# Kernel tuning notes

Measured on AMD Instinct MI355X. Metric: run time of the kernel, lower is better.

The kernel has to match this reference:

```python
import jax, jax.numpy as jnp
import numpy as np

N = 30000
E = 480000
F_IN = 16
HID = 64
HEADS = 2
D = HID // HEADS
L = 2
NEG_SLOPE = 0.2


def _edge_softmax(alpha, dst, num_nodes):
    # alpha: [E, HEADS]; softmax over edges sharing the same destination node
    amax = jax.ops.segment_max(alpha, dst, num_segments=num_nodes)
    ex = jnp.exp(alpha - amax[dst])
    den = jax.ops.segment_sum(ex, dst, num_segments=num_nodes)
    return ex / (den[dst] + 1e-16)


def _han_edge(x_src, x_dst, ei, a_src, a_dst, n_dst):
    # x_src: [N_src, HEADS, D], x_dst: [N_dst, HEADS, D], ei: [2, E]
    src, dst = ei[0], ei[1]
    a_s = jnp.einsum('nhd,hd->nh', x_src, a_src)
    a_d = jnp.einsum('nhd,hd->nh', x_dst, a_dst)
    alpha = jax.nn.leaky_relu(a_s[src] + a_d[dst], NEG_SLOPE)  # [E, HEADS]
    alpha = _edge_softmax(alpha, dst, n_dst)
    msg = x_src[src] * alpha[..., None]                        # [E, HEADS, D]
    out = jax.ops.segment_sum(msg, dst, num_segments=n_dst)
    return jax.nn.relu(out.reshape(n_dst, HID))


def _group(xs, q, kw, kb):
    # semantic (cross-relation) attention; xs: list of [N, HID]
    out = jnp.stack(xs)                           # [T, N, HID]
    k = jnp.tanh(out @ kw + kb).mean(axis=1)      # [T, HID]
    attn = jax.nn.softmax(jnp.einsum('f,tf->t', q, k))
    return jnp.einsum('t,tnf->nf', attn, out)


def setup_inputs() -> dict:
    key = jax.random.key(0)
    ks = jax.random.split(key, 24)
    s = 0.1
    f32 = jnp.float32
    return {
        'x_job': jax.random.normal(ks[0], (N, F_IN), f32),
        'x_machine': jax.random.normal(ks[1], (N, F_IN), f32),
        'edge_index_jm': jax.random.randint(ks[2], (2, E), 0, N),
        'edge_index_mj': jax.random.randint(ks[3], (2, E), 0, N),
        'edge_index_jj': jax.random.randint(ks[4], (2, E), 0, N),
        'enc_w_job': jax.random.normal(ks[5], (F_IN, HID), f32) * s,
        'enc_b_job': jax.random.normal(ks[6], (HID,), f32) * s,
        'enc_w_machine': jax.random.normal(ks[7], (F_IN, HID), f32) * s,
        'enc_b_machine': jax.random.normal(ks[8], (HID,), f32) * s,
        'proj_w': jax.random.normal(ks[9], (L, 2, HID, HID), f32) * s,
        'proj_b': jax.random.normal(ks[10], (L, 2, HID), f32) * s,
        'att_src': jax.random.normal(ks[11], (L, 3, HEADS, D), f32) * s,
        'att_dst': jax.random.normal(ks[12], (L, 3, HEADS, D), f32) * s,
        'klin_w': jax.random.normal(ks[13], (L, HID, HID), f32) * s,
        'klin_b': jax.random.normal(ks[14], (L, HID), f32) * s,
        'q_sem': jax.random.normal(ks[15], (L, HID), f32) * s,
        'lin0_w': jax.random.normal(ks[16], (HID, HID), f32) * s,
        'lin0_b': jax.random.normal(ks[17], (HID,), f32) * s,
        'linout_w': jax.random.normal(ks[18], (HID, 16), f32) * s,
        'linout_b': jax.random.normal(ks[19], (16,), f32) * s,
        'linv_w': jax.random.normal(ks[20], (HID, 1), f32) * s,
        'linv_b': jax.random.normal(ks[21], (1,), f32) * s,
    }


def reference(x_job, x_machine, edge_index_jm, edge_index_mj, edge_index_jj,
              enc_w_job, enc_b_job, enc_w_machine, enc_b_machine,
              proj_w, proj_b, att_src, att_dst, klin_w, klin_b, q_sem,
              lin0_w, lin0_b, linout_w, linout_b, linv_w, linv_b):
    # per-node-type encoder: Linear + relu_
    xj = jax.nn.relu(x_job @ enc_w_job + enc_b_job)          # [N, HID]
    xm = jax.nn.relu(x_machine @ enc_w_machine + enc_b_machine)
    for l in range(L):
        pj = (xj @ proj_w[l, 0] + proj_b[l, 0]).reshape(N, HEADS, D)
        pm = (xm @ proj_w[l, 1] + proj_b[l, 1]).reshape(N, HEADS, D)
        # edge-type order follows edge_index_dict iteration: jm, mj, jj
        out_jm = _han_edge(pj, pm, edge_index_jm, att_src[l, 0], att_dst[l, 0], N)
        out_mj = _han_edge(pm, pj, edge_index_mj, att_src[l, 1], att_dst[l, 1], N)
        out_jj = _han_edge(pj, pj, edge_index_jj, att_src[l, 2], att_dst[l, 2], N)
        xj = _group([out_mj, out_jj], q_sem[l], klin_w[l], klin_b[l])
        xm = _group([out_jm], q_sem[l], klin_w[l], klin_b[l])
    full_x = jnp.concatenate([xj, xm], axis=0)               # [2N, HID]
    value = (full_x @ linv_w + linv_b).mean()
    h = full_x @ lin0_w + lin0_b
    action = jnp.tanh(h @ linout_w + linout_b)               # [2N, 16]
    return action, value
```

## Files before the change

kernel.cpp:

```cpp
#include <hip/hip_runtime.h>
#include <math.h>


#define GEMM_GRID 1024
#define KRED_GRID 256
#define BUCKET_SHIFT 6
#define BUCKET_NODES 64
#define BUCKET_CAP 1536
#define BIN_CHUNK 2048

__device__ __forceinline__ float4 ld4(const float* __restrict__ p, int idx4)
{
    return ((const float4*)p)[idx4];
}

__device__ __forceinline__ float halfred(float v)
{
#pragma unroll
    for (int off = 16; off; off >>= 1) v += __shfl_xor(v, off);
    return v;
}

__device__ __forceinline__ float2 sem_attn(const float* __restrict__ kacc,
                                           const float* __restrict__ qsem,
                                           float inv_n, int lane)
{
    float qc = qsem[lane];
    float v0 = qc * kacc[lane] * inv_n;
    float v1 = qc * kacc[64 + lane] * inv_n;
#pragma unroll
    for (int off = 32; off; off >>= 1) {
        v0 += __shfl_xor(v0, off);
        v1 += __shfl_xor(v1, off);
    }
    float m = fmaxf(v0, v1);
    float e0 = __expf(v0 - m), e1 = __expf(v1 - m);
    float inv = 1.f / (e0 + e1);
    return {e0 * inv, e1 * inv};
}

struct ProjSide {
    const float* x0; const float* x1;
    const float* kacc; const float* qsem; float inv_n;
    const float* W; const float* b; float* p;
    const float* a0v; float* o0; const float* a1v; float* o1;
    const float* a2v; float* o2; const float* a3v; float* o3;
};

__global__ __launch_bounds__(256, 4) void proj2_kernel(ProjSide sa, ProjSide sb, int n)
{
    const ProjSide S = blockIdx.y ? sb : sa;
    __shared__ __align__(16) float xs[16][64];
    int tid = threadIdx.x, lane = tid & 63, wid = tid >> 6;
    float Wreg[64];
#pragma unroll
    for (int k = 0; k < 64; k++) Wreg[k] = S.W[k * 64 + lane];
    float bc = S.b[lane];
    float a0c = S.o0 ? S.a0v[lane] : 0.f;
    float a1c = S.o1 ? S.a1v[lane] : 0.f;
    float a2c = S.o2 ? S.a2v[lane] : 0.f;
    float a3c = S.o3 ? S.a3v[lane] : 0.f;
    float ca0 = 0.f, ca1 = 0.f;
    if (S.x1) {
        float2 at = sem_attn(S.kacc, S.qsem, S.inv_n, lane);
        ca0 = at.x; ca1 = at.y;
    }
    int qn = tid >> 4, qq = tid & 15;
    for (int base = blockIdx.x * 16; base < n; base += gridDim.x * 16) {
        __syncthreads();
        int node = base + qn;
        if (node < n) {
            float4 xq;
            if (S.x1) {
                float4 u = ld4(S.x0, node * 16 + qq), v = ld4(S.x1, node * 16 + qq);
                xq.x = ca0 * u.x + ca1 * v.x; xq.y = ca0 * u.y + ca1 * v.y;
                xq.z = ca0 * u.z + ca1 * v.z; xq.w = ca0 * u.w + ca1 * v.w;
            } else {
                xq = ld4(S.x0, node * 16 + qq);
            }
            *(float4*)&xs[qn][qq * 4] = xq;
        }
        __syncthreads();
#pragma unroll
        for (int nd = 0; nd < 4; nd++) {
            int nc = base + wid * 4 + nd;
            if (nc >= n) break;
            float acc = bc;
#pragma unroll
            for (int k4 = 0; k4 < 16; k4++) {
                float4 xv = *(const float4*)&xs[wid * 4 + nd][k4 * 4];
                acc = fmaf(xv.x, Wreg[4 * k4 + 0], acc);
                acc = fmaf(xv.y, Wreg[4 * k4 + 1], acc);
                acc = fmaf(xv.z, Wreg[4 * k4 + 2], acc);
                acc = fmaf(xv.w, Wreg[4 * k4 + 3], acc);
            }
            S.p[nc * 64 + lane] = acc;
            int h = lane >> 5;
            if (S.o0) { float v = halfred(acc * a0c); if ((lane & 31) == 0) S.o0[nc * 2 + h] = v; }
            if (S.o1) { float v = halfred(acc * a1c); if ((lane & 31) == 0) S.o1[nc * 2 + h] = v; }
            if (S.o2) { float v = halfred(acc * a2c); if ((lane & 31) == 0) S.o2[nc * 2 + h] = v; }
            if (S.o3) { float v = halfred(acc * a3c); if ((lane & 31) == 0) S.o3[nc * 2 + h] = v; }
        }
    }
}

struct EncSide {
    const float* x; const float* We; const float* be;
    const float* W; const float* b; float* p;
    const float* a0v; float* o0; const float* a1v; float* o1;
    const float* a2v; float* o2; const float* a3v; float* o3;
};

__global__ __launch_bounds__(256, 4) void encproj2_kernel(EncSide sa, EncSide sb, int n)
{
    const EncSide S = blockIdx.y ? sb : sa;
    __shared__ __align__(16) float xs[16][16];
    __shared__ __align__(16) float es[16][64];
    int tid = threadIdx.x, lane = tid & 63, wid = tid >> 6;
    float Ereg[16];
#pragma unroll
    for (int k = 0; k < 16; k++) Ereg[k] = S.We[k * 64 + lane];
    float Wreg[64];
#pragma unroll
    for (int k = 0; k < 64; k++) Wreg[k] = S.W[k * 64 + lane];
    float ebc = S.be[lane], bc = S.b[lane];
    float a0c = S.o0 ? S.a0v[lane] : 0.f;
    float a1c = S.o1 ? S.a1v[lane] : 0.f;
    float a2c = S.o2 ? S.a2v[lane] : 0.f;
    float a3c = S.o3 ? S.a3v[lane] : 0.f;
    for (int base = blockIdx.x * 16; base < n; base += gridDim.x * 16) {
        __syncthreads();
        if (tid < 64) {
            int nn = tid >> 2, q = tid & 3;
            int node = base + nn;
            if (node < n) *(float4*)&xs[nn][q * 4] = ld4(S.x, node * 4 + q);
        }
        __syncthreads();
#pragma unroll
        for (int nd = 0; nd < 4; nd++) {
            int nc = base + wid * 4 + nd;
            if (nc >= n) break;
            float a = ebc;
#pragma unroll
            for (int k4 = 0; k4 < 4; k4++) {
                float4 xv = *(const float4*)&xs[wid * 4 + nd][k4 * 4];
                a = fmaf(xv.x, Ereg[4 * k4 + 0], a);
                a = fmaf(xv.y, Ereg[4 * k4 + 1], a);
                a = fmaf(xv.z, Ereg[4 * k4 + 2], a);
                a = fmaf(xv.w, Ereg[4 * k4 + 3], a);
            }
            es[wid * 4 + nd][lane] = fmaxf(a, 0.f);
        }
        __syncthreads();
#pragma unroll
        for (int nd = 0; nd < 4; nd++) {
            int nc = base + wid * 4 + nd;
            if (nc >= n) break;
            float acc = bc;
#pragma unroll
            for (int k4 = 0; k4 < 16; k4++) {
                float4 xv = *(const float4*)&es[wid * 4 + nd][k4 * 4];
                acc = fmaf(xv.x, Wreg[4 * k4 + 0], acc);
                acc = fmaf(xv.y, Wreg[4 * k4 + 1], acc);
                acc = fmaf(xv.z, Wreg[4 * k4 + 2], acc);
                acc = fmaf(xv.w, Wreg[4 * k4 + 3], acc);
            }
            S.p[nc * 64 + lane] = acc;
            int h = lane >> 5;
            if (S.o0) { float v = halfred(acc * a0c); if ((lane & 31) == 0) S.o0[nc * 2 + h] = v; }
            if (S.o1) { float v = halfred(acc * a1c); if ((lane & 31) == 0) S.o1[nc * 2 + h] = v; }
            if (S.o2) { float v = halfred(acc * a2c); if ((lane & 31) == 0) S.o2[nc * 2 + h] = v; }
            if (S.o3) { float v = halfred(acc * a3c); if ((lane & 31) == 0) S.o3[nc * 2 + h] = v; }
        }
    }
}

__global__ __launch_bounds__(256) void bin_kernel(
    const int* __restrict__ s0, const int* __restrict__ s1, const int* __restrict__ s2,
    const int* __restrict__ d0, const int* __restrict__ d1, const int* __restrict__ d2,
    int* __restrict__ cursor, int* __restrict__ binned, int e, int nb)
{
    int ty = blockIdx.y;
    const int* s = ty == 0 ? s0 : (ty == 1 ? s1 : s2);
    const int* d = ty == 0 ? d0 : (ty == 1 ? d1 : d2);
    __shared__ int cnt[512], rbase[512];
    int tid = threadIdx.x;
    for (int i = tid; i < nb; i += 256) cnt[i] = 0;
    __syncthreads();
    int beg = blockIdx.x * BIN_CHUNK;
    int end = beg + BIN_CHUNK; if (end > e) end = e;
    for (int i = beg + tid; i < end; i += 256)
        atomicAdd(&cnt[d[i] >> BUCKET_SHIFT], 1);
    __syncthreads();
    for (int i = tid; i < nb; i += 256) {
        rbase[i] = atomicAdd(&cursor[ty * nb + i], cnt[i]);
        cnt[i] = 0;
    }
    __syncthreads();
    int* bb = binned + (size_t)ty * nb * BUCKET_CAP;
    for (int i = beg + tid; i < end; i += 256) {
        int dv = d[i], b = dv >> BUCKET_SHIFT;
        int slot = rbase[b] + atomicAdd(&cnt[b], 1);
        if (slot < BUCKET_CAP)
            bb[b * BUCKET_CAP + slot] = (s[i] << BUCKET_SHIFT) | (dv & (BUCKET_NODES - 1));
    }
}

__global__ void bucketscan_kernel(const int* __restrict__ cursor,
                                  int* __restrict__ bbase, int nb)
{
    int ty = blockIdx.x;
    const int* c = cursor + (size_t)ty * nb;
    int* o = bbase + (size_t)ty * nb;
    int lane = threadIdx.x;
    int carry = 0;
    for (int base = 0; base < nb; base += 64) {
        int i = base + lane;
        int v = (i < nb) ? c[i] : 0;
        int incl = v;
#pragma unroll
        for (int off = 1; off < 64; off <<= 1) {
            int u = __shfl_up(incl, off);
            if (lane >= off) incl += u;
        }
        if (i < nb) o[i] = carry + incl - v;
        carry += __shfl(incl, 63);
    }
}

__global__ __launch_bounds__(256) void bucket_kernel(
    const int* __restrict__ cursor, const int* __restrict__ bbase,
    const int* __restrict__ binned,
    int* __restrict__ rowptr, int* __restrict__ rowend, int* __restrict__ colsrc,
    int n, int nb, int e)
{
    int ty = blockIdx.y, b = blockIdx.x;
    __shared__ int stage[BUCKET_CAP];
    __shared__ int ncnt[64], nexcl[64], ncur[64];
    int tid = threadIdx.x;
    int cnt = cursor[ty * nb + b]; if (cnt > BUCKET_CAP) cnt = BUCKET_CAP;
    int base = bbase[ty * nb + b];
    const int* bb = binned + ((size_t)ty * nb + b) * BUCKET_CAP;
    if (tid < 64) ncnt[tid] = 0;
    __syncthreads();
    for (int i = tid; i < cnt; i += 256) {
        int v = bb[i];
        stage[i] = v;
        atomicAdd(&ncnt[v & (BUCKET_NODES - 1)], 1);
    }
    __syncthreads();
    if (tid < 64) {
        int v = ncnt[tid];
        int incl = v;
#pragma unroll
        for (int off = 1; off < 64; off <<= 1) {
            int u = __shfl_up(incl, off);
            if (tid >= off) incl += u;
        }
        int excl = incl - v;
        nexcl[tid] = excl;
        ncur[tid] = 0;
        int node = (b << BUCKET_SHIFT) + tid;
        if (node < n) {
            rowptr[(size_t)ty * n + node] = base + excl;
            rowend[(size_t)ty * n + node] = base + excl + v;
        }
    }
    __syncthreads();
    int* cs = colsrc + (size_t)ty * e;
    for (int i = tid; i < cnt; i += 256) {
        int v = stage[i];
        int dl = v & (BUCKET_NODES - 1);
        int pos = nexcl[dl] + atomicAdd(&ncur[dl], 1);
        cs[base + pos] = v >> BUCKET_SHIFT;
    }
}

struct AggSide {
    const int* rp; const int* re; const int* cs;
    const float* xsrc; const float* as; const float* ad;
    float* out;
};

__global__ __launch_bounds__(256, 8) void agg3_kernel(AggSide A0, AggSide A1, AggSide A2, int n)
{
    const AggSide A = blockIdx.y == 0 ? A0 : (blockIdx.y == 1 ? A1 : A2);
    __shared__ int ebs[4][32];
    __shared__ float ebw[4][2][32];
    int tid = threadIdx.x;
    int lane = tid & 63, wid = tid >> 6;
    int node = blockIdx.x * 4 + wid;
    if (node >= n) return;
    int l32 = lane & 31;
    int hh = lane >> 5;
    int g = lane >> 4;
    int q = lane & 15;
    int hq = q >> 3;
    int beg = A.rp[node], end = A.re[node];
    float ad = A.ad[node * 2 + hh];
    float den = 0.f;
    float4 acc = {0.f, 0.f, 0.f, 0.f};
    int* es = ebs[wid];
    float* ew = ebw[wid][0];
    for (int c = beg; c < end; c += 32) {
        int cnt = end - c; if (cnt > 32) cnt = 32;
        int sl = A.cs[c + (l32 < cnt ? l32 : 0)];
        float w = 0.f;
        if (l32 < cnt) {
            float a = A.as[sl * 2 + hh] + ad;
            a = (a > 0.f) ? a : 0.2f * a;
            w = __expf(a);
        }
        den += w;
        if (lane < 32) es[l32] = sl;
        ew[hh * 32 + l32] = w;
        int iters = (cnt + 3) >> 2;
        int it = 0;
        for (; it + 4 <= iters; it += 4) {
            int e0 = it * 4 + g;
            int s0 = es[e0], s1 = es[e0 + 4], s2 = es[e0 + 8], s3 = es[e0 + 12];
            float w0 = ew[hq * 32 + e0],     w1 = ew[hq * 32 + e0 + 4];
            float w2 = ew[hq * 32 + e0 + 8], w3 = ew[hq * 32 + e0 + 12];
            float4 x0 = ld4(A.xsrc, s0 * 16 + q);
            float4 x1 = ld4(A.xsrc, s1 * 16 + q);
            float4 x2 = ld4(A.xsrc, s2 * 16 + q);
            float4 x3 = ld4(A.xsrc, s3 * 16 + q);
            acc.x = fmaf(w0, x0.x, acc.x); acc.y = fmaf(w0, x0.y, acc.y);
            acc.z = fmaf(w0, x0.z, acc.z); acc.w = fmaf(w0, x0.w, acc.w);
            acc.x = fmaf(w1, x1.x, acc.x); acc.y = fmaf(w1, x1.y, acc.y);
            acc.z = fmaf(w1, x1.z, acc.z); acc.w = fmaf(w1, x1.w, acc.w);
            acc.x = fmaf(w2, x2.x, acc.x); acc.y = fmaf(w2, x2.y, acc.y);
            acc.z = fmaf(w2, x2.z, acc.z); acc.w = fmaf(w2, x2.w, acc.w);
            acc.x = fmaf(w3, x3.x, acc.x); acc.y = fmaf(w3, x3.y, acc.y);
            acc.z = fmaf(w3, x3.z, acc.z); acc.w = fmaf(w3, x3.w, acc.w);
        }
        for (; it < iters; it++) {
            int e0 = it * 4 + g;
            int s0 = es[e0];
            float w0 = ew[hq * 32 + e0];
            float4 x0 = ld4(A.xsrc, s0 * 16 + q);
            acc.x = fmaf(w0, x0.x, acc.x); acc.y = fmaf(w0, x0.y, acc.y);
            acc.z = fmaf(w0, x0.z, acc.z); acc.w = fmaf(w0, x0.w, acc.w);
        }
    }
    acc.x += __shfl_xor(acc.x, 16);
    acc.y += __shfl_xor(acc.y, 16);
    acc.z += __shfl_xor(acc.z, 16);
    acc.w += __shfl_xor(acc.w, 16);
    acc.x += __shfl_xor(acc.x, 32);
    acc.y += __shfl_xor(acc.y, 32);
    acc.z += __shfl_xor(acc.z, 32);
    acc.w += __shfl_xor(acc.w, 32);
    float dtot = halfred(den);
    float dq = __shfl(dtot, (q >= 8) ? 32 : 0);
    if (g == 0) {
        float r = 1.f / (dq + 1e-16f);
        float4 o;
        o.x = fmaxf(acc.x * r, 0.f);
        o.y = fmaxf(acc.y * r, 0.f);
        o.z = fmaxf(acc.z * r, 0.f);
        o.w = fmaxf(acc.w * r, 0.f);
        *(float4*)&A.out[node * 64 + q * 4] = o;
    }
}

__global__ __launch_bounds__(256, 4) void kred2_kernel(
    const float* __restrict__ xin0, const float* __restrict__ xin1,
    const float* __restrict__ kw, const float* __restrict__ kb,
    float* __restrict__ kacc0, float* __restrict__ kacc1, int n)
{
    const float* xin = blockIdx.y ? xin1 : xin0;
    float* kacc = blockIdx.y ? kacc1 : kacc0;
    __shared__ __align__(16) float xs[16][64];
    __shared__ float red[256];
    int tid = threadIdx.x, lane = tid & 63, wid = tid >> 6;
    float Wreg[64];
#pragma unroll
    for (int k = 0; k < 64; k++) Wreg[k] = kw[k * 64 + lane];
    float bc = kb[lane];
    int qn = tid >> 4, qq = tid & 15;
    float kl = 0.f;
    for (int base = blockIdx.x * 16; base < n; base += gridDim.x * 16) {
        __syncthreads();
        int node = base + qn;
        if (node < n) *(float4*)&xs[qn][qq * 4] = ld4(xin, node * 16 + qq);
        __syncthreads();
#pragma unroll
        for (int nd = 0; nd < 4; nd++) {
            int nc = base + wid * 4 + nd;
            if (nc >= n) break;
            float acc = bc;
#pragma unroll
            for (int k4 = 0; k4 < 16; k4++) {
                float4 xv = *(const float4*)&xs[wid * 4 + nd][k4 * 4];
                acc = fmaf(xv.x, Wreg[4 * k4 + 0], acc);
                acc = fmaf(xv.y, Wreg[4 * k4 + 1], acc);
                acc = fmaf(xv.z, Wreg[4 * k4 + 2], acc);
                acc = fmaf(xv.w, Wreg[4 * k4 + 3], acc);
            }
            kl += tanhf(acc);
        }
    }
    red[tid] = kl;
    __syncthreads();
    if (wid == 0) {
        float s = red[lane] + red[64 + lane] + red[128 + lane] + red[192 + lane];
        atomicAdd(&kacc[lane], s);
    }
}

__global__ __launch_bounds__(256, 4) void final_kernel(
    const float* __restrict__ t0, const float* __restrict__ t1,
    const float* __restrict__ kacc, const float* __restrict__ qsem, float inv_n,
    const float* __restrict__ xm,
    const float* __restrict__ w0, const float* __restrict__ b0,
    const float* __restrict__ w1, const float* __restrict__ b1,
    const float* __restrict__ wv,
    float* __restrict__ action, float* __restrict__ vsum, int n)
{
    __shared__ __align__(16) float xs[16][64];
    __shared__ __align__(16) float hs[4][4][68];
    __shared__ float W1s[1024];
    __shared__ float red[256];
    int tid = threadIdx.x, lane = tid & 63, wid = tid >> 6;
    int qn = tid >> 4, qq = tid & 15;
    float W0reg[64];
#pragma unroll
    for (int k = 0; k < 64; k++) W0reg[k] = w0[k * 64 + lane];
    float b0c = b0[lane], b1c = b1[lane & 15];
    float2 at = sem_attn(kacc, qsem, inv_n, lane);
    float ca0 = at.x, ca1 = at.y;
    float4 wvq = ld4(wv, qq);
    for (int i = tid; i < 1024; i += 256) W1s[i] = w1[i];
    float vloc = 0.f;
    int n2 = 2 * n;
    for (int base = blockIdx.x * 16; base < n2; base += gridDim.x * 16) {
        __syncthreads();
        int node = base + qn;
        if (node < n2) {
            float4 xq;
            if (node < n) {
                float4 u = ld4(t0, node * 16 + qq), v = ld4(t1, node * 16 + qq);
                xq.x = ca0 * u.x + ca1 * v.x; xq.y = ca0 * u.y + ca1 * v.y;
                xq.z = ca0 * u.z + ca1 * v.z; xq.w = ca0 * u.w + ca1 * v.w;
            } else {
                xq = ld4(xm, (node - n) * 16 + qq);
            }
            *(float4*)&xs[qn][qq * 4] = xq;
            vloc += xq.x * wvq.x + xq.y * wvq.y + xq.z * wvq.z + xq.w * wvq.w;
        }
        __syncthreads();
#pragma unroll
        for (int nd = 0; nd < 4; nd++) {
            int nc = base + wid * 4 + nd;
            if (nc >= n2) break;
            float acc = b0c;
#pragma unroll
            for (int k4 = 0; k4 < 16; k4++) {
                float4 xv = *(const float4*)&xs[wid * 4 + nd][k4 * 4];
                acc = fmaf(xv.x, W0reg[4 * k4 + 0], acc);
                acc = fmaf(xv.y, W0reg[4 * k4 + 1], acc);
                acc = fmaf(xv.z, W0reg[4 * k4 + 2], acc);
                acc = fmaf(xv.w, W0reg[4 * k4 + 3], acc);
            }
            hs[wid][nd][lane] = acc;
        }
        __syncthreads();
        int nd2 = lane >> 4, c2 = lane & 15;
        int nc2 = base + wid * 4 + nd2;
        if (nc2 < n2) {
            float acc2 = b1c;
#pragma unroll
            for (int k4 = 0; k4 < 16; k4++) {
                float4 hv = *(const float4*)&hs[wid][nd2][k4 * 4];
                acc2 = fmaf(hv.x, W1s[(4 * k4 + 0) * 16 + c2], acc2);
                acc2 = fmaf(hv.y, W1s[(4 * k4 + 1) * 16 + c2], acc2);
                acc2 = fmaf(hv.z, W1s[(4 * k4 + 2) * 16 + c2], acc2);
                acc2 = fmaf(hv.w, W1s[(4 * k4 + 3) * 16 + c2], acc2);
            }
            action[(size_t)nc2 * 16 + c2] = tanhf(acc2);
        }
    }
    red[tid] = vloc;
    __syncthreads();
    for (int s = 128; s; s >>= 1) {
        if (tid < s) red[tid] += red[tid + s];
        __syncthreads();
    }
    if (tid == 0) atomicAdd(vsum, red[0]);
}

__global__ void value_finish_kernel(const float* __restrict__ vsum,
                                    const float* __restrict__ vb,
                                    float* __restrict__ out, int twoN)
{
    if (threadIdx.x == 0 && blockIdx.x == 0)
        out[0] = vsum[0] / (float)twoN + vb[0];
}

extern "C" void kernel_launch(void* const* d_in, const int* in_sizes, int n_in,
                              void* d_out, int out_size, void* d_ws, size_t ws_size,
                              hipStream_t stream)
{
    const int N = in_sizes[0] / 16;
    const int E = in_sizes[2] / 2;
    const int NB = (N + BUCKET_NODES - 1) / BUCKET_NODES;

    auto f = [&](int i) { return (const float*)d_in[i]; };
    const float* x_job = f(0);
    const float* x_mac = f(1);
    const int* ei_jm = (const int*)d_in[2];
    const int* ei_mj = (const int*)d_in[3];
    const int* ei_jj = (const int*)d_in[4];
    const float* enc_wj = f(5);
    const float* enc_bj = f(6);
    const float* enc_wm = f(7);
    const float* enc_bm = f(8);
    const float* proj_w = f(9);
    const float* proj_b = f(10);
    const float* att_src = f(11);
    const float* att_dst = f(12);
    const float* klin_w = f(13);
    const float* klin_b = f(14);
    const float* q_sem = f(15);
    const float* lin0_w = f(16);
    const float* lin0_b = f(17);
    const float* lout_w = f(18);
    const float* lout_b = f(19);
    const float* linv_w = f(20);
    const float* linv_b = f(21);

    float* action = (float*)d_out;
    float* value_out = action + (size_t)2 * N * 16;

    char* base = (char*)d_ws;
    size_t off = 0;
    auto alloc = [&](size_t bytes) -> void* {
        void* p = base + off;
        off += (bytes + 255) & ~(size_t)255;
        return p;
    };
    int* cursor3 = (int*)alloc((size_t)3 * NB * 4);
    float* kacc = (float*)alloc(256 * 4);
    float* vsum = (float*)alloc(4);
    size_t zero_bytes = off;

    int* bbase3 = (int*)alloc((size_t)3 * NB * 4);
    int* rowptr3 = (int*)alloc((size_t)3 * N * 4);
    int* rowend3 = (int*)alloc((size_t)3 * N * 4);
    int* colsrc3 = (int*)alloc((size_t)3 * E * 4);
    float* pj = (float*)alloc((size_t)N * 64 * 4);
    float* pm = (float*)alloc((size_t)N * 64 * 4);
    float* out_jm0 = (float*)alloc((size_t)N * 64 * 4);
    float* out_jm1 = (float*)alloc((size_t)N * 64 * 4);
    float* out_mj = (float*)alloc((size_t)N * 64 * 4);
    float* out_jj = (float*)alloc((size_t)N * 64 * 4);
    float* as_jm = (float*)alloc((size_t)N * 2 * 4);
    float* ad_jm = (float*)alloc((size_t)N * 2 * 4);
    float* as_mj = (float*)alloc((size_t)N * 2 * 4);
    float* ad_mj = (float*)alloc((size_t)N * 2 * 4);
    float* as_jj = (float*)alloc((size_t)N * 2 * 4);
    float* ad_jj = (float*)alloc((size_t)N * 2 * 4);

    int* binned3 = (int*)pj;

    hipMemsetAsync(d_ws, 0, zero_bytes, stream);

    dim3 blk(256);

    int nchunks = (E + BIN_CHUNK - 1) / BIN_CHUNK;
    bin_kernel<<<dim3(nchunks, 3), blk, 0, stream>>>(
        ei_jm, ei_mj, ei_jj, ei_jm + E, ei_mj + E, ei_jj + E,
        cursor3, binned3, E, NB);
    bucketscan_kernel<<<3, 64, 0, stream>>>(cursor3, bbase3, NB);
    bucket_kernel<<<dim3(NB, 3), blk, 0, stream>>>(
        cursor3, bbase3, binned3, rowptr3, rowend3, colsrc3, N, NB, E);

    const int* rp0 = rowptr3;
    const int* rp1 = rowptr3 + N;
    const int* rp2 = rowptr3 + 2 * N;
    const int* re0 = rowend3;
    const int* re1 = rowend3 + N;
    const int* re2 = rowend3 + 2 * N;
    const int* cs0 = colsrc3;
    const int* cs1 = colsrc3 + E;
    const int* cs2 = colsrc3 + 2 * E;

    int ab = (N + 3) / 4;
    float* out_jm_l[2] = {out_jm0, out_jm1};
    float inv_n = 1.f / (float)N;

    for (int l = 0; l < 2; l++) {
        const float* pwj = proj_w + (size_t)(l * 2 + 0) * 4096;
        const float* pwm = proj_w + (size_t)(l * 2 + 1) * 4096;
        const float* pbj = proj_b + (l * 2 + 0) * 64;
        const float* pbm = proj_b + (l * 2 + 1) * 64;
        const float* as0 = att_src + (l * 3 + 0) * 64;
        const float* as1 = att_src + (l * 3 + 1) * 64;
        const float* as2 = att_src + (l * 3 + 2) * 64;
        const float* ad0 = att_dst + (l * 3 + 0) * 64;
        const float* ad1 = att_dst + (l * 3 + 1) * 64;
        const float* ad2 = att_dst + (l * 3 + 2) * 64;

        if (l == 0) {
            EncSide ja = {x_job, enc_wj, enc_bj, pwj, pbj, pj,
                          as0, as_jm, ad1, ad_mj, as2, as_jj, ad2, ad_jj};
            EncSide ma = {x_mac, enc_wm, enc_bm, pwm, pbm, pm,
                          ad0, ad_jm, as1, as_mj, nullptr, nullptr, nullptr, nullptr};
            encproj2_kernel<<<dim3(GEMM_GRID, 2), blk, 0, stream>>>(ja, ma, N);
        } else {
            ProjSide ja = {out_mj, out_jj, kacc, q_sem, inv_n, pwj, pbj, pj,
                           as0, as_jm, ad1, ad_mj, as2, as_jj, ad2, ad_jj};
            ProjSide ma = {out_jm0, nullptr, nullptr, nullptr, 0.f, pwm, pbm, pm,
                           ad0, ad_jm, as1, as_mj, nullptr, nullptr, nullptr, nullptr};
            proj2_kernel<<<dim3(GEMM_GRID, 2), blk, 0, stream>>>(ja, ma, N);
        }

        AggSide A0 = {rp0, re0, cs0, pj, as_jm, ad_jm, out_jm_l[l]};
        AggSide A1 = {rp1, re1, cs1, pm, as_mj, ad_mj, out_mj};
        AggSide A2 = {rp2, re2, cs2, pj, as_jj, ad_jj, out_jj};
        agg3_kernel<<<dim3(ab, 3), blk, 0, stream>>>(A0, A1, A2, N);

        const float* kw = klin_w + (size_t)l * 4096;
        const float* kb = klin_b + l * 64;
        float* k0 = kacc + l * 128;
        float* k1 = k0 + 64;
        kred2_kernel<<<dim3(KRED_GRID, 2), blk, 0, stream>>>(out_mj, out_jj, kw, kb, k0, k1, N);
    }

    final_kernel<<<GEMM_GRID * 2, blk, 0, stream>>>(out_mj, out_jj,
                                                    kacc + 128, q_sem + 64, inv_n,
                                                    out_jm1,
                                                    lin0_w, lin0_b, lout_w, lout_b, linv_w,
                                                    action, vsum, N);
    value_finish_kernel<<<1, 64, 0, stream>>>(vsum, linv_b, value_out, 2 * N);
}
```

Measured before the change: 361.0 us.

## Merge edge binning into encoder kernel and fold bucket scan into bucket kernel

```diff
diff --git a/kernel.cpp b/kernel.cpp
--- a/kernel.cpp
+++ b/kernel.cpp
@@ -3,6 +3,7 @@
 
 
 #define GEMM_GRID 1024
+#define ENCB 1024
 #define KRED_GRID 256
 #define BUCKET_SHIFT 6
 #define BUCKET_NODES 64
@@ -111,9 +112,8 @@
     const float* a2v; float* o2; const float* a3v; float* o3;
 };
 
-__global__ __launch_bounds__(256, 4) void encproj2_kernel(EncSide sa, EncSide sb, int n)
-{
-    const EncSide S = blockIdx.y ? sb : sa;
+__device__ __forceinline__ void encproj_body(const EncSide& S, int bx, int nblk, int n)
+{
     __shared__ __align__(16) float xs[16][16];
     __shared__ __align__(16) float es[16][64];
     int tid = threadIdx.x, lane = tid & 63, wid = tid >> 6;
@@ -128,7 +128,7 @@
     float a1c = S.o1 ? S.a1v[lane] : 0.f;
     float a2c = S.o2 ? S.a2v[lane] : 0.f;
     float a3c = S.o3 ? S.a3v[lane] : 0.f;
-    for (int base = blockIdx.x * 16; base < n; base += gridDim.x * 16) {
+    for (int base = bx * 16; base < n; base += nblk * 16) {
         __syncthreads();
         if (tid < 64) {
             int nn = tid >> 2, q = tid & 3;
@@ -175,19 +175,15 @@
     }
 }
 
-__global__ __launch_bounds__(256) void bin_kernel(
-    const int* __restrict__ s0, const int* __restrict__ s1, const int* __restrict__ s2,
-    const int* __restrict__ d0, const int* __restrict__ d1, const int* __restrict__ d2,
-    int* __restrict__ cursor, int* __restrict__ binned, int e, int nb)
-{
-    int ty = blockIdx.y;
-    const int* s = ty == 0 ? s0 : (ty == 1 ? s1 : s2);
-    const int* d = ty == 0 ? d0 : (ty == 1 ? d1 : d2);
+__device__ __forceinline__ void bin_body(const int* __restrict__ s, const int* __restrict__ d,
+                                         int* __restrict__ cursor, int* __restrict__ binned,
+                                         int ty, int cx, int e, int nb)
+{
     __shared__ int cnt[512], rbase[512];
     int tid = threadIdx.x;
     for (int i = tid; i < nb; i += 256) cnt[i] = 0;
     __syncthreads();
-    int beg = blockIdx.x * BIN_CHUNK;
+    int beg = cx * BIN_CHUNK;
     int end = beg + BIN_CHUNK; if (end > e) end = e;
     for (int i = beg + tid; i < end; i += 256)
         atomicAdd(&cnt[d[i] >> BUCKET_SHIFT], 1);
@@ -206,43 +202,44 @@
     }
 }
 
-__global__ void bucketscan_kernel(const int* __restrict__ cursor,
-                                  int* __restrict__ bbase, int nb)
-{
-    int ty = blockIdx.x;
-    const int* c = cursor + (size_t)ty * nb;
-    int* o = bbase + (size_t)ty * nb;
-    int lane = threadIdx.x;
-    int carry = 0;
-    for (int base = 0; base < nb; base += 64) {
-        int i = base + lane;
-        int v = (i < nb) ? c[i] : 0;
-        int incl = v;
-#pragma unroll
-        for (int off = 1; off < 64; off <<= 1) {
-            int u = __shfl_up(incl, off);
-            if (lane >= off) incl += u;
-        }
-        if (i < nb) o[i] = carry + incl - v;
-        carry += __shfl(incl, 63);
+__global__ __launch_bounds__(256) void phase1_kernel(
+    EncSide sa, EncSide sb, int n,
+    const int* __restrict__ s0, const int* __restrict__ s1, const int* __restrict__ s2,
+    const int* __restrict__ d0, const int* __restrict__ d1, const int* __restrict__ d2,
+    int* __restrict__ cursor, int* __restrict__ binned, int e, int nb, int binb)
+{
+    int bid = blockIdx.x;
+    if (bid < 2 * ENCB) {
+        encproj_body(bid >= ENCB ? sb : sa, bid & (ENCB - 1), ENCB, n);
+    } else {
+        int r = bid - 2 * ENCB;
+        int ty = r / binb, cx = r % binb;
+        const int* s = ty == 0 ? s0 : (ty == 1 ? s1 : s2);
+        const int* d = ty == 0 ? d0 : (ty == 1 ? d1 : d2);
+        bin_body(s, d, cursor, binned, ty, cx, e, nb);
     }
 }
 
 __global__ __launch_bounds__(256) void bucket_kernel(
-    const int* __restrict__ cursor, const int* __restrict__ bbase,
-    const int* __restrict__ binned,
+    const int* __restrict__ cursor, const int* __restrict__ binned,
     int* __restrict__ rowptr, int* __restrict__ rowend, int* __restrict__ colsrc,
     int n, int nb, int e)
 {
     int ty = blockIdx.y, b = blockIdx.x;
     __shared__ int stage[BUCKET_CAP];
     __shared__ int ncnt[64], nexcl[64], ncur[64];
-    int tid = threadIdx.x;
+    __shared__ int wpart[4];
+    int tid = threadIdx.x, lane = tid & 63, wid = tid >> 6;
+    int part = 0;
+    for (int i = tid; i < b; i += 256) part += cursor[ty * nb + i];
+#pragma unroll
+    for (int off = 32; off; off >>= 1) part += __shfl_xor(part, off);
+    if (lane == 0) wpart[wid] = part;
     int cnt = cursor[ty * nb + b]; if (cnt > BUCKET_CAP) cnt = BUCKET_CAP;
-    int base = bbase[ty * nb + b];
     const int* bb = binned + ((size_t)ty * nb + b) * BUCKET_CAP;
     if (tid < 64) ncnt[tid] = 0;
     __syncthreads();
+    int base = wpart[0] + wpart[1] + wpart[2] + wpart[3];
     for (int i = tid; i < cnt; i += 256) {
         int v = bb[i];
         stage[i] = v;
@@ -545,10 +542,10 @@
     float* vsum = (float*)alloc(4);
     size_t zero_bytes = off;
 
-    int* bbase3 = (int*)alloc((size_t)3 * NB * 4);
     int* rowptr3 = (int*)alloc((size_t)3 * N * 4);
     int* rowend3 = (int*)alloc((size_t)3 * N * 4);
     int* colsrc3 = (int*)alloc((size_t)3 * E * 4);
+    int* binned3 = (int*)alloc((size_t)3 * NB * BUCKET_CAP * 4);
     float* pj = (float*)alloc((size_t)N * 64 * 4);
     float* pm = (float*)alloc((size_t)N * 64 * 4);
     float* out_jm0 = (float*)alloc((size_t)N * 64 * 4);
@@ -562,19 +559,9 @@
     float* as_jj = (float*)alloc((size_t)N * 2 * 4);
     float* ad_jj = (float*)alloc((size_t)N * 2 * 4);
 
-    int* binned3 = (int*)pj;
-
     hipMemsetAsync(d_ws, 0, zero_bytes, stream);
 
     dim3 blk(256);
-
-    int nchunks = (E + BIN_CHUNK - 1) / BIN_CHUNK;
-    bin_kernel<<<dim3(nchunks, 3), blk, 0, stream>>>(
-        ei_jm, ei_mj, ei_jj, ei_jm + E, ei_mj + E, ei_jj + E,
-        cursor3, binned3, E, NB);
-    bucketscan_kernel<<<3, 64, 0, stream>>>(cursor3, bbase3, NB);
-    bucket_kernel<<<dim3(NB, 3), blk, 0, stream>>>(
-        cursor3, bbase3, binned3, rowptr3, rowend3, colsrc3, N, NB, E);
 
     const int* rp0 = rowptr3;
     const int* rp1 = rowptr3 + N;
@@ -587,6 +574,7 @@
     const int* cs2 = colsrc3 + 2 * E;
 
     int ab = (N + 3) / 4;
+    int binb = (E + BIN_CHUNK - 1) / BIN_CHUNK;
     float* out_jm_l[2] = {out_jm0, out_jm1};
     float inv_n = 1.f / (float)N;
 
@@ -607,7 +595,11 @@
                           as0, as_jm, ad1, ad_mj, as2, as_jj, ad2, ad_jj};
             EncSide ma = {x_mac, enc_wm, enc_bm, pwm, pbm, pm,
                           ad0, ad_jm, as1, as_mj, nullptr, nullptr, nullptr, nullptr};
-            encproj2_kernel<<<dim3(GEMM_GRID, 2), blk, 0, stream>>>(ja, ma, N);
+            phase1_kernel<<<2 * ENCB + 3 * binb, blk, 0, stream>>>(
+                ja, ma, N, ei_jm, ei_mj, ei_jj, ei_jm + E, ei_mj + E, ei_jj + E,
+                cursor3, binned3, E, NB, binb);
+            bucket_kernel<<<dim3(NB, 3), blk, 0, stream>>>(
+                cursor3, binned3, rowptr3, rowend3, colsrc3, N, NB, E);
         } else {
             ProjSide ja = {out_mj, out_jj, kacc, q_sem, inv_n, pwj, pbj, pj,
                            as0, as_jm, ad1, ad_mj, as2, as_jj, ad2, ad_jj};
```

After: 352.0 us. -2.5%, faster.
